# Optimization experiments

Hardware: AMD Instinct MI355X
Metric: run time of the kernel (lower is better)

## Reference

```python
import jax, jax.numpy as jnp
import numpy as np

DIM = 96
HEADS = 6
HEAD_DIM = DIM // HEADS  # 16
WIN = 8
N = WIN * WIN            # 64
C = 4 * DIM              # 384
TABLE = (2 * WIN - 1) ** 2  # 225


def setup_inputs() -> dict:
    key = jax.random.key(0)
    ks = jax.random.split(key, 12)
    B_ = 2048  # num_windows * batch = 1024 * 2
    NW = 1024
    x = jax.random.normal(ks[0], (B_, N, C), dtype=jnp.float32)
    cross_x = jax.random.normal(ks[1], (B_, N, C), dtype=jnp.float32)
    rpi = jax.random.randint(ks[2], (N, N), 0, TABLE)
    mask = jnp.zeros((NW, N, N), dtype=jnp.float32)
    s = 0.02
    Wq = jax.random.normal(ks[3], (C, DIM), dtype=jnp.float32) * s
    bq = jnp.zeros((DIM,), dtype=jnp.float32)
    Wk = jax.random.normal(ks[4], (C, DIM), dtype=jnp.float32) * s
    bk = jnp.zeros((DIM,), dtype=jnp.float32)
    Wv = jax.random.normal(ks[5], (C, C), dtype=jnp.float32) * s
    bv = jnp.zeros((C,), dtype=jnp.float32)
    Wp = jax.random.normal(ks[6], (C, C), dtype=jnp.float32) * s
    bp = jnp.zeros((C,), dtype=jnp.float32)
    rpb_table = jax.random.normal(ks[7], (TABLE, HEADS), dtype=jnp.float32) * 0.02
    return {"x": x, "cross_x": cross_x, "rpi": rpi, "mask": mask,
            "Wq": Wq, "bq": bq, "Wk": Wk, "bk": bk, "Wv": Wv, "bv": bv,
            "Wp": Wp, "bp": bp, "rpb_table": rpb_table}


def reference(x, cross_x, rpi, mask, Wq, bq, Wk, bk, Wv, bv, Wp, bp, rpb_table):
    b_, n, c = x.shape
    scale = HEAD_DIM ** (-0.5)
    # projections: q,k -> dim; v -> c (=4*dim)
    q = (x @ Wq + bq).reshape(b_, n, HEADS, HEAD_DIM).transpose(0, 2, 1, 3)
    k = (cross_x @ Wk + bk).reshape(b_, n, HEADS, HEAD_DIM).transpose(0, 2, 1, 3)
    v = (cross_x @ Wv + bv).reshape(b_, n, HEADS, c // HEADS).transpose(0, 2, 1, 3)
    attn = jnp.einsum('bhnd,bhmd->bhnm', q * scale, k)
    # relative position bias: gather (n*n,) indices -> (n, n, heads) -> (heads, n, n)
    bias = rpb_table[rpi.reshape(-1)].reshape(n, n, HEADS).transpose(2, 0, 1)
    attn = attn + bias[None]
    nw = mask.shape[0]
    attn = attn.reshape(b_ // nw, nw, HEADS, n, n) + mask[None, :, None]
    attn = attn.reshape(b_, HEADS, n, n)
    attn = jax.nn.softmax(attn, axis=-1)
    out = jnp.einsum('bhnm,bhmd->bhnd', attn, v)  # (b_, heads, n, c//heads)
    out = out.transpose(0, 2, 1, 3).reshape(b_, n, c)
    out = out @ Wp + bp
    return out
```

## Files before the change

### kernel.cpp

```cpp
#include <hip/hip_runtime.h>
#include <hip/hip_bf16.h>


typedef __attribute__((ext_vector_type(8))) short short8;
typedef __attribute__((ext_vector_type(4))) float f32x4;

__device__ __forceinline__ f32x4 mfma_b16(short8 a, short8 b, f32x4 c) {
  return __builtin_amdgcn_mfma_f32_16x16x32_bf16(a, b, c, 0, 0, 0);
}

__device__ __forceinline__ unsigned short f2bf(float x) {
  return __builtin_bit_cast(unsigned short, __float2bfloat16(x));
}

__device__ __forceinline__ unsigned pack2(float a, float b) {
  return (unsigned)f2bf(a) | ((unsigned)f2bf(b) << 16);
}

__device__ __forceinline__ int swz48(int c, int r) {
  return (c & ~7) | ((c ^ r) & 7);
}

__device__ __forceinline__ void gl_lds16(const char* g, char* l) {
  __builtin_amdgcn_global_load_lds(
      (const __attribute__((address_space(1))) unsigned int*)g,
      (__attribute__((address_space(3))) unsigned int*)l, 16, 0, 0);
}

__global__ void prep_k(const float* __restrict__ Wq, const float* __restrict__ Wk,
                       const float* __restrict__ Wv, const float* __restrict__ Wp,
                       const float* __restrict__ rpb, const int* __restrict__ rpi,
                       const float* __restrict__ bk, const float* __restrict__ bv,
                       unsigned short* __restrict__ Wq_t, unsigned short* __restrict__ Wkv_t,
                       unsigned short* __restrict__ Wp_t, float* __restrict__ bias6,
                       float* __restrict__ bias_kv) {
  const int T0 = 96 * 384, T1 = 480 * 384, T2 = 384 * 384, T3 = 6 * 4096, T4 = 480;
  int total = T0 + T1 + T2 + T3 + T4;
  for (int i = blockIdx.x * blockDim.x + threadIdx.x; i < total;
       i += gridDim.x * blockDim.x) {
    int r = i;
    if (r < T0) {
      int n = r / 384, k = r % 384;
      Wq_t[r] = f2bf(Wq[k * 96 + n]);
    } else if ((r -= T0) < T1) {
      int n = r / 384, k = r % 384;
      Wkv_t[r] = f2bf(n < 96 ? Wk[k * 96 + n] : Wv[k * 384 + (n - 96)]);
    } else if ((r -= T1) < T2) {
      int n = r / 384, k = r % 384;
      Wp_t[r] = f2bf(Wp[k * 384 + n]);
    } else if ((r -= T2) < T3) {
      int h = r >> 12, ij = r & 4095;
      bias6[r] = rpb[rpi[ij] * 6 + h];
    } else {
      r -= T3;
      bias_kv[r] = (r < 96) ? bk[r] : bv[r - 96];
    }
  }
}

template <int A_MODE, int OUT_MODE, int NX>
__global__ __launch_bounds__(256, 4) void gemm3_k(
    const void* __restrict__ Av, const unsigned short* __restrict__ Bt,
    const float* __restrict__ bias, void* __restrict__ Outv,
    unsigned short* __restrict__ k_out, unsigned short* __restrict__ vt_out) {
  __shared__ char lds[40960];
  constexpr int AB[2] = {0, 8192}, BB[2] = {16384, 28672};
  const int tid = threadIdx.x, lane = tid & 63, wid = tid >> 6;
  const int g = blockIdx.x;
  const int lg_id = (g & 7) * (NX * 256) + (g >> 3);
  const int my = lg_id / NX, nx = lg_id - my * NX;
  const int m0 = my * 64, n0 = nx * 96;
  const int wm = (wid >> 1) * 32, wn = (wid & 1) * 48;
  const int lr = lane & 15, lg = lane >> 4;

  float4 areg[4];
  const int ar = tid >> 2, aq = tid & 3;

  auto a_issue_f32 = [&](int kt) {
    const float* A = (const float*)Av + (size_t)(m0 + ar) * 384 + kt * 64 + aq * 16;
#pragma unroll
    for (int p = 0; p < 4; ++p) areg[p] = *reinterpret_cast<const float4*>(A + p * 4);
  };
  auto a_write_f32 = [&](char* Ab) {
    unsigned pk[8];
#pragma unroll
    for (int p = 0; p < 4; ++p) {
      pk[p * 2]     = pack2(areg[p].x, areg[p].y);
      pk[p * 2 + 1] = pack2(areg[p].z, areg[p].w);
    }
    const int c0 = aq * 2;
    *reinterpret_cast<uint4*>(Ab + ar * 128 + ((c0 ^ (ar & 7)) * 16)) =
        make_uint4(pk[0], pk[1], pk[2], pk[3]);
    *reinterpret_cast<uint4*>(Ab + ar * 128 + (((c0 + 1) ^ (ar & 7)) * 16)) =
        make_uint4(pk[4], pk[5], pk[6], pk[7]);
  };
  auto b_issue = [&](int kt, char* Bb) {
#pragma unroll
    for (int j = 0; j < 3; ++j) {
      const int rb = (wid * 3 + j) * 8;
      const int row = rb + (lane >> 3), c = lane & 7;
      gl_lds16((const char*)Bt + (size_t)(n0 + row) * 768 + kt * 128 +
                   ((c ^ (row & 7)) * 16),
               Bb + rb * 128);
    }
  };

  f32x4 acc[2][3];
#pragma unroll
  for (int i = 0; i < 2; ++i)
#pragma unroll
    for (int j = 0; j < 3; ++j) acc[i][j] = (f32x4){0.f, 0.f, 0.f, 0.f};

  a_issue_f32(0);
  a_write_f32(lds + AB[0]);
  b_issue(0, lds + BB[0]);
  __syncthreads();

  int cur = 0;
  for (int kt = 0; kt < 6; ++kt) {
    char* An = lds + AB[cur ^ 1];
    char* Bn = lds + BB[cur ^ 1];
    if (kt < 5) {
      a_issue_f32(kt + 1);
      b_issue(kt + 1, Bn);
    }
    {
      const char* Ab = lds + AB[cur];
      const char* Bb = lds + BB[cur];
#pragma unroll
      for (int ks = 0; ks < 2; ++ks) {
        short8 a[2], b[3];
#pragma unroll
        for (int mf = 0; mf < 2; ++mf) {
          const int row = wm + mf * 16 + lr;
          a[mf] = *reinterpret_cast<const short8*>(
              Ab + row * 128 + (((ks * 4 + lg) ^ (row & 7)) * 16));
        }
#pragma unroll
        for (int nf = 0; nf < 3; ++nf) {
          const int row = wn + nf * 16 + lr;
          b[nf] = *reinterpret_cast<const short8*>(
              Bb + row * 128 + (((ks * 4 + lg) ^ (row & 7)) * 16));
        }
#pragma unroll
        for (int mf = 0; mf < 2; ++mf)
#pragma unroll
          for (int nf = 0; nf < 3; ++nf)
            acc[mf][nf] = mfma_b16(a[mf], b[nf], acc[mf][nf]);
      }
    }
    if (kt < 5) a_write_f32(An);
    __syncthreads();
    cur ^= 1;
  }

  if (OUT_MODE == 0 || (OUT_MODE == 2 && nx == 0)) {
    unsigned short* dst = (OUT_MODE == 0) ? (unsigned short*)Outv : k_out;
#pragma unroll
    for (int mf = 0; mf < 2; ++mf)
#pragma unroll
      for (int nf = 0; nf < 3; ++nf) {
        const int col = wn + nf * 16 + lr;
        const float bb = bias[col];
#pragma unroll
        for (int r = 0; r < 4; ++r) {
          const int row = wm + mf * 16 + lg * 4 + r;
          *reinterpret_cast<unsigned short*>(lds + row * 208 + col * 2) =
              f2bf(acc[mf][nf][r] + bb);
        }
      }
    __syncthreads();
#pragma unroll
    for (int j = 0; j < 3; ++j) {
      const int Lb = (j * 256 + tid) * 16;
      const int row = Lb / 192, inner = Lb % 192;
      *reinterpret_cast<uint4*>((char*)dst + (size_t)(m0 + row) * 192 + inner) =
          *reinterpret_cast<const uint4*>(lds + row * 208 + inner);
    }
  } else {
#pragma unroll
    for (int mf = 0; mf < 2; ++mf)
#pragma unroll
      for (int nf = 0; nf < 3; ++nf) {
        const int dl = wn + nf * 16 + lr;
        const float bb = bias[n0 + dl];
        const int tok0 = wm + mf * 16 + lg * 4;
        *reinterpret_cast<unsigned*>(lds + dl * 144 + tok0 * 2) =
            pack2(acc[mf][nf][0] + bb, acc[mf][nf][1] + bb);
        *reinterpret_cast<unsigned*>(lds + dl * 144 + tok0 * 2 + 4) =
            pack2(acc[mf][nf][2] + bb, acc[mf][nf][3] + bb);
      }
    __syncthreads();
#pragma unroll
    for (int j = 0; j < 3; ++j) {
      const int Lc = j * 256 + tid;
      const int dl = Lc >> 3, c = Lc & 7;
      *reinterpret_cast<uint4*>((char*)vt_out + (size_t)my * 49152 +
                                (size_t)((nx - 1) * 96 + dl) * 128 +
                                ((c ^ (dl & 7)) << 4)) =
          *reinterpret_cast<const uint4*>(lds + dl * 144 + c * 16);
    }
  }
}

__global__ __launch_bounds__(256, 2) void ap_k(
    const unsigned short* __restrict__ q_buf, const unsigned short* __restrict__ k_buf,
    const unsigned short* __restrict__ vt_buf, const float* __restrict__ bias6,
    const float* __restrict__ mask, const unsigned short* __restrict__ Wp_t,
    const float* __restrict__ bp, float* __restrict__ out) {
  __shared__ char lds[81920];
  const int tid = threadIdx.x, lane = tid & 63, wid = tid >> 6;
  const int lr = lane & 15, lg = lane >> 4;
  const int w = blockIdx.x;

  auto b_issue = [&](int T, char* Bb) {
    const int nc = T / 6, kt = T - nc * 6;
#pragma unroll
    for (int j = 0; j < 3; ++j) {
      const int rb = (wid * 3 + j) * 8;
      const int row = rb + (lane >> 3), c = lane & 7;
      gl_lds16((const char*)Wp_t + (size_t)(nc * 96 + row) * 768 + kt * 128 +
                   ((c ^ (row & 7)) * 16),
               Bb + rb * 128);
    }
  };

  const char* vsrc = (const char*)vt_buf + (size_t)w * 49152;
#pragma unroll
  for (int j = 0; j < 12; ++j) {
    const int off = (wid * 12 + j) * 1024;
    gl_lds16(vsrc + off + lane * 16, lds + off);
  }
  b_issue(0, lds + 57344);
  b_issue(1, lds + 57344 + 12288);
  __syncthreads();

  unsigned stash[48];
  char* Plds = lds + 49152;
  const float* mw = mask + (size_t)(w & 1023) * 4096;
  const int iq = wid * 16 + lr;

  for (int h = 0; h < 6; ++h) {
    short8 qa = {0, 0, 0, 0, 0, 0, 0, 0};
    if (lg < 2)
      qa = *reinterpret_cast<const short8*>(
          q_buf + (size_t)(w * 64 + iq) * 96 + h * 16 + lg * 8);
    float sv[4][4];
#pragma unroll
    for (int tj = 0; tj < 4; ++tj) {
      short8 kf = {0, 0, 0, 0, 0, 0, 0, 0};
      if (lg < 2)
        kf = *reinterpret_cast<const short8*>(
            k_buf + (size_t)(w * 64 + tj * 16 + lr) * 96 + h * 16 + lg * 8);
      f32x4 z = {0.f, 0.f, 0.f, 0.f};
      f32x4 s = mfma_b16(kf, qa, z);
      const int j0 = tj * 16 + lg * 4;
      const float4 bi = *reinterpret_cast<const float4*>(bias6 + h * 4096 + iq * 64 + j0);
      const float4 mk = *reinterpret_cast<const float4*>(mw + iq * 64 + j0);
      sv[tj][0] = s[0] * 0.25f + bi.x + mk.x;
      sv[tj][1] = s[1] * 0.25f + bi.y + mk.y;
      sv[tj][2] = s[2] * 0.25f + bi.z + mk.z;
      sv[tj][3] = s[3] * 0.25f + bi.w + mk.w;
    }
    float mx = sv[0][0];
#pragma unroll
    for (int tj = 0; tj < 4; ++tj)
#pragma unroll
      for (int r = 0; r < 4; ++r) mx = fmaxf(mx, sv[tj][r]);
    mx = fmaxf(mx, __shfl_xor(mx, 16));
    mx = fmaxf(mx, __shfl_xor(mx, 32));
    float sum = 0.f;
#pragma unroll
    for (int tj = 0; tj < 4; ++tj)
#pragma unroll
      for (int r = 0; r < 4; ++r) {
        sv[tj][r] = __expf(sv[tj][r] - mx);
        sum += sv[tj][r];
      }
    sum += __shfl_xor(sum, 16);
    sum += __shfl_xor(sum, 32);
    const float inv = 1.0f / sum;
#pragma unroll
    for (int tj = 0; tj < 4; ++tj) {
      const int c = tj * 2 + (lg >> 1);
      uint2 st;
      st.x = pack2(sv[tj][0] * inv, sv[tj][1] * inv);
      st.y = pack2(sv[tj][2] * inv, sv[tj][3] * inv);
      *reinterpret_cast<uint2*>(Plds + iq * 128 + ((c ^ (iq & 7)) << 4) +
                                (lg & 1) * 8) = st;
    }
    short8 pa[2];
#pragma unroll
    for (int ks = 0; ks < 2; ++ks)
      pa[ks] = *reinterpret_cast<const short8*>(
          Plds + iq * 128 + (((ks * 4 + lg) ^ (iq & 7)) << 4));
#pragma unroll
    for (int td = 0; td < 4; ++td) {
      f32x4 o = {0.f, 0.f, 0.f, 0.f};
#pragma unroll
      for (int ks = 0; ks < 2; ++ks) {
        const int d = h * 64 + td * 16 + lr;
        short8 vb = *reinterpret_cast<const short8*>(
            lds + d * 128 + (((ks * 4 + lg) ^ (d & 7)) << 4));
        o = mfma_b16(vb, pa[ks], o);
      }
      stash[h * 8 + td * 2 + 0] = pack2(o[0], o[1]);
      stash[h * 8 + td * 2 + 1] = pack2(o[2], o[3]);
    }
  }
  __syncthreads();

#pragma unroll
  for (int h = 0; h < 6; ++h)
#pragma unroll
    for (int td = 0; td < 4; ++td)
#pragma unroll
      for (int p2 = 0; p2 < 2; ++p2) {
        const int c0 = h * 64 + td * 16 + lg * 4 + p2 * 2;
        *reinterpret_cast<unsigned*>(
            lds + iq * 768 + swz48(c0 >> 3, iq) * 16 + ((c0 * 2) & 15)) =
            stash[h * 8 + td * 2 + p2];
      }
  __syncthreads();

  const int wm = (wid >> 1) * 32, wn = (wid & 1) * 48;
  f32x4 acc[2][3];
#pragma unroll
  for (int i = 0; i < 2; ++i)
#pragma unroll
    for (int j = 0; j < 3; ++j) acc[i][j] = (f32x4){0.f, 0.f, 0.f, 0.f};

  for (int T = 0; T < 24; ++T) {
    const int nc = T / 6, kt = T - nc * 6;
    if (T >= 1 && T < 23) b_issue(T + 1, lds + 57344 + ((T + 1) & 1) * 12288);
    const char* Bb = lds + 57344 + (T & 1) * 12288;
#pragma unroll
    for (int ks = 0; ks < 2; ++ks) {
      short8 a[2], b[3];
#pragma unroll
      for (int mf = 0; mf < 2; ++mf) {
        const int row = wm + mf * 16 + lr;
        a[mf] = *reinterpret_cast<const short8*>(
            lds + row * 768 + swz48(kt * 8 + ks * 4 + lg, row) * 16);
      }
#pragma unroll
      for (int nf = 0; nf < 3; ++nf) {
        const int row = wn + nf * 16 + lr;
        b[nf] = *reinterpret_cast<const short8*>(
            Bb + row * 128 + (((ks * 4 + lg) ^ (row & 7)) * 16));
      }
#pragma unroll
      for (int mf = 0; mf < 2; ++mf)
#pragma unroll
        for (int nf = 0; nf < 3; ++nf)
          acc[mf][nf] = mfma_b16(a[mf], b[nf], acc[mf][nf]);
    }
    if (kt == 5) {
#pragma unroll
      for (int mf = 0; mf < 2; ++mf)
#pragma unroll
        for (int nf = 0; nf < 3; ++nf) {
          const int col = nc * 96 + wn + nf * 16 + lr;
          const float bb = bp[col];
#pragma unroll
          for (int r = 0; r < 4; ++r) {
            const int row = wm + mf * 16 + lg * 4 + r;
            out[(size_t)(w * 64 + row) * 384 + col] = acc[mf][nf][r] + bb;
          }
          acc[mf][nf] = (f32x4){0.f, 0.f, 0.f, 0.f};
        }
    }
    __syncthreads();
  }
}

extern "C" void kernel_launch(void* const* d_in, const int* in_sizes, int n_in,
                              void* d_out, int out_size, void* d_ws, size_t ws_size,
                              hipStream_t stream) {
  const float* x    = (const float*)d_in[0];
  const float* cx   = (const float*)d_in[1];
  const int*   rpi  = (const int*)d_in[2];
  const float* mask = (const float*)d_in[3];
  const float* Wq   = (const float*)d_in[4];
  const float* bq   = (const float*)d_in[5];
  const float* Wk   = (const float*)d_in[6];
  const float* bk   = (const float*)d_in[7];
  const float* Wv   = (const float*)d_in[8];
  const float* bv   = (const float*)d_in[9];
  const float* Wp   = (const float*)d_in[10];
  const float* bp   = (const float*)d_in[11];
  const float* rpb  = (const float*)d_in[12];

  char* ws = (char*)d_ws;
  unsigned short* Wq_t   = (unsigned short*)(ws + 0);
  unsigned short* Wkv_t  = (unsigned short*)(ws + 73728);
  unsigned short* Wp_t   = (unsigned short*)(ws + 442368);
  float*          bias6  = (float*)(ws + 737280);
  float*          biaskv = (float*)(ws + 835584);
  const size_t MB = 1u << 20;
  unsigned short* q_buf  = (unsigned short*)(ws + MB);
  unsigned short* k_buf  = (unsigned short*)(ws + MB + 25165824u);
  unsigned short* vt_buf = (unsigned short*)(ws + MB + 50331648u);

  prep_k<<<256, 256, 0, stream>>>(Wq, Wk, Wv, Wp, rpb, rpi, bk, bv,
                                  Wq_t, Wkv_t, Wp_t, bias6, biaskv);
  gemm3_k<0, 0, 1><<<2048, 256, 0, stream>>>(x, Wq_t, bq, q_buf, nullptr, nullptr);
  gemm3_k<0, 2, 5><<<10240, 256, 0, stream>>>(cx, Wkv_t, biaskv, nullptr, k_buf, vt_buf);
  ap_k<<<2048, 256, 0, stream>>>(q_buf, k_buf, vt_buf, bias6, mask, Wp_t, bp,
                                 (float*)d_out);
}
```

Before: 347.9 us.

## Shrink LDS in attention-projection kernel to raise occupancy with streamed V tiles

The fused attention+projection kernel now streams V per head into a double-buffered 16KB region instead of loading all of V at once. It also reworks the output projection so each wave owns its own 16 rows and stages its stashed attention output per k-tile through a small private LDS region, removing the full 64x384 staging buffer. Together these cut LDS from 80KB to 48KB and raise launch bounds to 3 blocks per CU. It also adds setprio around MFMA bursts and explicit waitcnt barriers per head. The cost is more barriers, more per-head synchronisation, and higher register pressure from 12 accumulators under a tighter register budget.

```diff
diff --git a/kernel.cpp b/kernel.cpp
--- a/kernel.cpp
+++ b/kernel.cpp
@@ -15,10 +15,6 @@
 
 __device__ __forceinline__ unsigned pack2(float a, float b) {
   return (unsigned)f2bf(a) | ((unsigned)f2bf(b) << 16);
-}
-
-__device__ __forceinline__ int swz48(int c, int r) {
-  return (c & ~7) | ((c ^ r) & 7);
 }
 
 __device__ __forceinline__ void gl_lds16(const char* g, char* l) {
@@ -26,6 +22,12 @@
       (const __attribute__((address_space(1))) unsigned int*)g,
       (__attribute__((address_space(3))) unsigned int*)l, 16, 0, 0);
 }
+
+#define HEADSYNC                                                      \
+  asm volatile("s_waitcnt vmcnt(0) lgkmcnt(0)" ::: "memory");         \
+  __builtin_amdgcn_sched_barrier(0);                                  \
+  __builtin_amdgcn_s_barrier();                                       \
+  __builtin_amdgcn_sched_barrier(0)
 
 __global__ void prep_k(const float* __restrict__ Wq, const float* __restrict__ Wk,
                        const float* __restrict__ Wv, const float* __restrict__ Wp,
@@ -203,18 +205,20 @@
   }
 }
 
-__global__ __launch_bounds__(256, 2) void ap_k(
+__global__ __launch_bounds__(256, 3) void ap_k(
     const unsigned short* __restrict__ q_buf, const unsigned short* __restrict__ k_buf,
     const unsigned short* __restrict__ vt_buf, const float* __restrict__ bias6,
     const float* __restrict__ mask, const unsigned short* __restrict__ Wp_t,
     const float* __restrict__ bp, float* __restrict__ out) {
-  __shared__ char lds[81920];
+  __shared__ char lds[49152];
   const int tid = threadIdx.x, lane = tid & 63, wid = tid >> 6;
   const int lr = lane & 15, lg = lane >> 4;
   const int w = blockIdx.x;
-
-  auto b_issue = [&](int T, char* Bb) {
-    const int nc = T / 6, kt = T - nc * 6;
+  char* Pr = lds + 16384;
+  char* Bbase = lds + 24576;
+  const char* vsrc = (const char*)vt_buf + (size_t)w * 49152;
+
+  auto b_issue = [&](int nc, int kt, char* Bb) {
 #pragma unroll
     for (int j = 0; j < 3; ++j) {
       const int rb = (wid * 3 + j) * 8;
@@ -224,23 +228,27 @@
                Bb + rb * 128);
     }
   };
-
-  const char* vsrc = (const char*)vt_buf + (size_t)w * 49152;
-#pragma unroll
-  for (int j = 0; j < 12; ++j) {
-    const int off = (wid * 12 + j) * 1024;
-    gl_lds16(vsrc + off + lane * 16, lds + off);
-  }
-  b_issue(0, lds + 57344);
-  b_issue(1, lds + 57344 + 12288);
+  auto v_issue = [&](int h, int buf) {
+    const char* src = vsrc + h * 8192 + wid * 2048 + lane * 16;
+    char* dst = lds + buf * 8192 + wid * 2048;
+    gl_lds16(src, dst);
+    gl_lds16(src + 1024, dst + 1024);
+  };
+
+  v_issue(0, 0);
+  b_issue(0, 0, Bbase);
+  b_issue(1, 0, Bbase + 12288);
   __syncthreads();
 
   unsigned stash[48];
-  char* Plds = lds + 49152;
   const float* mw = mask + (size_t)(w & 1023) * 4096;
   const int iq = wid * 16 + lr;
 
+#pragma unroll
   for (int h = 0; h < 6; ++h) {
+    if (h) { HEADSYNC; }
+    if (h < 5) v_issue(h + 1, (h + 1) & 1);
+
     short8 qa = {0, 0, 0, 0, 0, 0, 0, 0};
     if (lg < 2)
       qa = *reinterpret_cast<const short8*>(
@@ -286,91 +294,89 @@
       uint2 st;
       st.x = pack2(sv[tj][0] * inv, sv[tj][1] * inv);
       st.y = pack2(sv[tj][2] * inv, sv[tj][3] * inv);
-      *reinterpret_cast<uint2*>(Plds + iq * 128 + ((c ^ (iq & 7)) << 4) +
+      *reinterpret_cast<uint2*>(Pr + iq * 128 + ((c ^ (iq & 7)) << 4) +
                                 (lg & 1) * 8) = st;
     }
     short8 pa[2];
 #pragma unroll
     for (int ks = 0; ks < 2; ++ks)
       pa[ks] = *reinterpret_cast<const short8*>(
-          Plds + iq * 128 + (((ks * 4 + lg) ^ (iq & 7)) << 4));
+          Pr + iq * 128 + (((ks * 4 + lg) ^ (iq & 7)) << 4));
+    __builtin_amdgcn_s_setprio(1);
 #pragma unroll
     for (int td = 0; td < 4; ++td) {
       f32x4 o = {0.f, 0.f, 0.f, 0.f};
 #pragma unroll
       for (int ks = 0; ks < 2; ++ks) {
-        const int d = h * 64 + td * 16 + lr;
+        const int dr = td * 16 + lr;
         short8 vb = *reinterpret_cast<const short8*>(
-            lds + d * 128 + (((ks * 4 + lg) ^ (d & 7)) << 4));
+            lds + (h & 1) * 8192 + dr * 128 + (((ks * 4 + lg) ^ (dr & 7)) << 4));
         o = mfma_b16(vb, pa[ks], o);
       }
       stash[h * 8 + td * 2 + 0] = pack2(o[0], o[1]);
       stash[h * 8 + td * 2 + 1] = pack2(o[2], o[3]);
     }
+    __builtin_amdgcn_s_setprio(0);
   }
-  __syncthreads();
-
-#pragma unroll
-  for (int h = 0; h < 6; ++h)
-#pragma unroll
-    for (int td = 0; td < 4; ++td)
-#pragma unroll
-      for (int p2 = 0; p2 < 2; ++p2) {
-        const int c0 = h * 64 + td * 16 + lg * 4 + p2 * 2;
-        *reinterpret_cast<unsigned*>(
-            lds + iq * 768 + swz48(c0 >> 3, iq) * 16 + ((c0 * 2) & 15)) =
-            stash[h * 8 + td * 2 + p2];
-      }
-  __syncthreads();
-
-  const int wm = (wid >> 1) * 32, wn = (wid & 1) * 48;
-  f32x4 acc[2][3];
-#pragma unroll
-  for (int i = 0; i < 2; ++i)
-#pragma unroll
-    for (int j = 0; j < 3; ++j) acc[i][j] = (f32x4){0.f, 0.f, 0.f, 0.f};
-
-  for (int T = 0; T < 24; ++T) {
-    const int nc = T / 6, kt = T - nc * 6;
-    if (T >= 1 && T < 23) b_issue(T + 1, lds + 57344 + ((T + 1) & 1) * 12288);
-    const char* Bb = lds + 57344 + (T & 1) * 12288;
-#pragma unroll
-    for (int ks = 0; ks < 2; ++ks) {
-      short8 a[2], b[3];
-#pragma unroll
-      for (int mf = 0; mf < 2; ++mf) {
-        const int row = wm + mf * 16 + lr;
-        a[mf] = *reinterpret_cast<const short8*>(
-            lds + row * 768 + swz48(kt * 8 + ks * 4 + lg, row) * 16);
-      }
-#pragma unroll
-      for (int nf = 0; nf < 3; ++nf) {
-        const int row = wn + nf * 16 + lr;
-        b[nf] = *reinterpret_cast<const short8*>(
-            Bb + row * 128 + (((ks * 4 + lg) ^ (row & 7)) * 16));
-      }
-#pragma unroll
-      for (int mf = 0; mf < 2; ++mf)
-#pragma unroll
-        for (int nf = 0; nf < 3; ++nf)
-          acc[mf][nf] = mfma_b16(a[mf], b[nf], acc[mf][nf]);
-    }
-    if (kt == 5) {
-#pragma unroll
-      for (int mf = 0; mf < 2; ++mf)
-#pragma unroll
-        for (int nf = 0; nf < 3; ++nf) {
-          const int col = nc * 96 + wn + nf * 16 + lr;
-          const float bb = bp[col];
-#pragma unroll
-          for (int r = 0; r < 4; ++r) {
-            const int row = wm + mf * 16 + lg * 4 + r;
-            out[(size_t)(w * 64 + row) * 384 + col] = acc[mf][nf][r] + bb;
+
+#pragma unroll 1
+  for (int P = 0; P < 2; ++P) {
+    f32x4 acc[2][6];
+#pragma unroll
+    for (int i = 0; i < 2; ++i)
+#pragma unroll
+      for (int j = 0; j < 6; ++j) acc[i][j] = (f32x4){0.f, 0.f, 0.f, 0.f};
+
+#pragma unroll
+    for (int kt = 0; kt < 6; ++kt) {
+#pragma unroll
+      for (int td = 0; td < 4; ++td) {
+        uint2 st = make_uint2(stash[kt * 8 + td * 2], stash[kt * 8 + td * 2 + 1]);
+        *reinterpret_cast<uint2*>(
+            Pr + iq * 128 + (((td * 2 + (lg >> 1)) ^ (iq & 7)) << 4) +
+            (lg & 1) * 8) = st;
+      }
+      short8 a0 = *reinterpret_cast<const short8*>(
+          Pr + iq * 128 + (((0 * 4 + lg) ^ (iq & 7)) << 4));
+      short8 a1 = *reinterpret_cast<const short8*>(
+          Pr + iq * 128 + (((1 * 4 + lg) ^ (iq & 7)) << 4));
+
+#pragma unroll
+      for (int ncl = 0; ncl < 2; ++ncl) {
+        const int T = P * 12 + kt * 2 + ncl;
+        if (T >= 1 && T < 23) {
+          const int Tn = T + 1;
+          const int Pn = Tn / 12, rem = Tn - Pn * 12;
+          b_issue(Pn * 2 + (rem & 1), rem >> 1, Bbase + (Tn & 1) * 12288);
+        }
+        const char* Bb = Bbase + (T & 1) * 12288;
+        __builtin_amdgcn_s_setprio(1);
+#pragma unroll
+        for (int ks = 0; ks < 2; ++ks) {
+          const short8 a = ks ? a1 : a0;
+#pragma unroll
+          for (int nf = 0; nf < 6; ++nf) {
+            const int row = nf * 16 + lr;
+            const short8 b = *reinterpret_cast<const short8*>(
+                Bb + row * 128 + (((ks * 4 + lg) ^ (row & 7)) * 16));
+            acc[ncl][nf] = mfma_b16(a, b, acc[ncl][nf]);
           }
-          acc[mf][nf] = (f32x4){0.f, 0.f, 0.f, 0.f};
         }
-    }
-    __syncthreads();
+        __builtin_amdgcn_s_setprio(0);
+        __syncthreads();
+      }
+    }
+#pragma unroll
+    for (int ncl = 0; ncl < 2; ++ncl)
+#pragma unroll
+      for (int nf = 0; nf < 6; ++nf) {
+        const int col = (P * 2 + ncl) * 96 + nf * 16 + lr;
+        const float bb = bp[col];
+#pragma unroll
+        for (int r = 0; r < 4; ++r)
+          out[(size_t)(w * 64 + wid * 16 + lg * 4 + r) * 384 + col] =
+              acc[ncl][nf][r] + bb;
+      }
   }
 }
 
```

New measurement: 361.8 us. 1.04x slower.
